# Performance work log

Measured on AMD Instinct MI355X. Metric: run time of the kernel, lower is better.

Reference implementation:

```python
import jax, jax.numpy as jnp
import numpy as np

ATTN_SPLITS = 2
TEMPERATURE = 10000.0

# ---------- split / merge helpers (faithful to split_feature / merge_splits) ----------

def split_cf(x, ns):  # channel-first [b,c,h,w] -> [b*ns*ns, c, h/ns, w/ns]
    b, c, h, w = x.shape
    x = x.reshape(b, c, ns, h // ns, ns, w // ns).transpose(0, 2, 4, 1, 3, 5)
    return x.reshape(b * ns * ns, c, h // ns, w // ns)

def merge_cf(x, ns):  # channel-first inverse
    b, c, h, w = x.shape
    nb = b // (ns * ns)
    x = x.reshape(nb, ns, ns, c, h, w).transpose(0, 3, 1, 4, 2, 5)
    return x.reshape(nb, c, ns * h, ns * w)

def split_cl(x, ns):  # channel-last [b,h,w,c] -> [b*ns*ns, h/ns, w/ns, c]
    b, h, w, c = x.shape
    x = x.reshape(b, ns, h // ns, ns, w // ns, c).transpose(0, 1, 3, 2, 4, 5)
    return x.reshape(b * ns * ns, h // ns, w // ns, c)

def merge_cl(x, ns):  # channel-last inverse
    b, h, w, c = x.shape
    nb = b // (ns * ns)
    x = x.reshape(nb, ns, ns, h, w, c).transpose(0, 1, 3, 2, 4, 5)
    return x.reshape(nb, ns * h, ns * w, c)

# ---------- PositionEmbeddingSine (normalize=True, scale=2*pi) ----------

def pos_embed_sine(h, w, num_pos_feats):
    scale = 2.0 * np.pi
    eps = 1e-6
    ones = jnp.ones((h, w), jnp.float32)
    y_embed = jnp.cumsum(ones, 0)
    x_embed = jnp.cumsum(ones, 1)
    y_embed = y_embed / (y_embed[-1:, :] + eps) * scale
    x_embed = x_embed / (x_embed[:, -1:] + eps) * scale
    dim_t = jnp.arange(num_pos_feats, dtype=jnp.float32)
    dim_t = TEMPERATURE ** (2.0 * jnp.floor(dim_t / 2.0) / num_pos_feats)
    pos_x = x_embed[:, :, None] / dim_t  # [h,w,npf]
    pos_y = y_embed[:, :, None] / dim_t
    pos_x = jnp.stack([jnp.sin(pos_x[:, :, 0::2]), jnp.cos(pos_x[:, :, 1::2])], -1).reshape(h, w, -1)
    pos_y = jnp.stack([jnp.sin(pos_y[:, :, 0::2]), jnp.cos(pos_y[:, :, 1::2])], -1).reshape(h, w, -1)
    pos = jnp.concatenate([pos_y, pos_x], -1)  # [h,w,c]
    return jnp.transpose(pos, (2, 0, 1))[None]  # [1,c,h,w]

def feature_add_position(f0, f1, attn_splits, c):
    if attn_splits > 1:
        f0s = split_cf(f0, attn_splits)
        f1s = split_cf(f1, attn_splits)
        pos = pos_embed_sine(f0s.shape[2], f0s.shape[3], c // 2)
        return merge_cf(f0s + pos, attn_splits), merge_cf(f1s + pos, attn_splits)
    pos = pos_embed_sine(f0.shape[2], f0.shape[3], c // 2)
    return f0 + pos, f1 + pos

# ---------- shifted-window attention mask (static, numpy) ----------

def shift_window_attn_mask(h, w, ns):
    wsh, wsw = h // ns, w // ns
    ssh, ssw = wsh // 2, wsw // 2
    img = np.zeros((h, w), np.float32)
    cnt = 0
    for hs in (slice(0, -wsh), slice(-wsh, -ssh), slice(-ssh, None)):
        for ws in (slice(0, -wsw), slice(-wsw, -ssw), slice(-ssw, None)):
            img[hs, ws] = cnt
            cnt += 1
    m = img.reshape(ns, wsh, ns, wsw).transpose(0, 2, 1, 3).reshape(ns * ns, wsh * wsw)
    am = m[:, None, :] - m[:, :, None]
    am = np.where(am != 0, -100.0, 0.0).astype(np.float32)
    return jnp.asarray(am)  # [ns*ns, N, N]

# ---------- single-head split (shifted) window attention ----------

def split_window_attention(q, k, v, ns, h, w, attn_mask):
    b, _, c = q.shape
    bn = b * ns * ns
    wsh, wsw = h // ns, w // ns
    ssh, ssw = wsh // 2, wsw // 2
    q = q.reshape(b, h, w, c)
    k = k.reshape(b, h, w, c)
    v = v.reshape(b, h, w, c)
    q = jnp.roll(q, (-ssh, -ssw), (1, 2))
    k = jnp.roll(k, (-ssh, -ssw), (1, 2))
    v = jnp.roll(v, (-ssh, -ssw), (1, 2))
    qs = split_cl(q, ns).reshape(bn, -1, c)
    ks = split_cl(k, ns).reshape(bn, -1, c)
    vs = split_cl(v, ns).reshape(bn, -1, c)
    scores = jnp.einsum('bnc,bmc->bnm', qs, ks) / jnp.sqrt(jnp.asarray(c, qs.dtype))
    scores = scores + jnp.tile(attn_mask, (b, 1, 1))
    attn = jax.nn.softmax(scores, axis=-1)
    out = jnp.einsum('bnm,bmc->bnc', attn, vs)
    out = merge_cl(out.reshape(bn, wsh, wsw, c), ns)
    out = jnp.roll(out, (ssh, ssw), (1, 2))
    return out.reshape(b, -1, c)

# ---------- global correlation softmax matching ----------

def global_correlation_softmax(f0, f1):
    b, c, h, w = f0.shape
    f0v = f0.reshape(b, c, -1)  # [b,c,hw]
    f1v = f1.reshape(b, c, -1)
    corr = jnp.einsum('bcn,bcm->bnm', f0v, f1v) / jnp.sqrt(jnp.asarray(c, f0.dtype))
    yy, xx = jnp.meshgrid(jnp.arange(h), jnp.arange(w), indexing='ij')
    grid = jnp.stack([xx, yy], 0).astype(f0.dtype)  # [2,h,w] (x,y)
    gridv = grid.reshape(2, -1).T  # [hw,2]
    prob = jax.nn.softmax(corr, axis=-1)
    corresp = jnp.einsum('bnm,md->bnd', prob, gridv).reshape(b, h, w, 2).transpose(0, 3, 1, 2)
    flow = corresp - grid[None]
    return flow

# ---------- setup & reference ----------

def setup_inputs() -> dict:
    key = jax.random.key(0)
    k0, k1 = jax.random.split(key)
    b, c, h, w = 4, 128, 64, 64
    feature0 = jax.random.normal(k0, (b, c, h, w), jnp.float32)
    feature1 = jax.random.normal(k1, (b, c, h, w), jnp.float32)
    return {'feature0': feature0, 'feature1': feature1}

def reference(feature0, feature1):
    b, c, h, w = feature0.shape
    ns = ATTN_SPLITS
    f0, f1 = feature_add_position(feature0, feature1, ns, c)
    attn_mask = shift_window_attn_mask(h, w, ns)
    q = f0.reshape(b, c, -1).transpose(0, 2, 1)  # [b,hw,c]
    kv = f1.reshape(b, c, -1).transpose(0, 2, 1)
    f0_attn = split_window_attention(q, kv, kv, ns, h, w, attn_mask)  # [b,hw,c]
    f0_attn = f0_attn.transpose(0, 2, 1).reshape(b, c, h, w)
    flow = global_correlation_softmax(f0_attn, f1)  # [b,2,h,w]
    return flow
```

## Files before the change

### kernel.cpp

```cpp
#include <hip/hip_runtime.h>
#include <hip/hip_bf16.h>
#include <math.h>

#define NB 4
#define NC 128
#define NH 64
#define NW 64
#define NHW 4096
#define SCALE 0.08838834764831845f

typedef short bf16x8 __attribute__((ext_vector_type(8)));
typedef float f32x4 __attribute__((ext_vector_type(4)));

__device__ __forceinline__ unsigned bfbits(float f) {
    unsigned u = __float_as_uint(f);
    return (u + 0x7FFFu + ((u >> 16) & 1u)) >> 16;
}
__device__ __forceinline__ unsigned bfpair(float a, float b) {
    return bfbits(a) | (bfbits(b) << 16);
}

__device__ __forceinline__ float posval(int c, int yy, int xx) {
    const float twopi_over_denom = 6.283185307179586f / (32.0f + 1e-6f);
    const int cc = (c < 64) ? c : (c - 64);
    const float e = (float)(((c < 64) ? yy : xx) + 1) * twopi_over_denom;
    const int k = cc >> 1;
    const float arg = e * exp2f(-0.41524101186091903f * (float)k);
    return (cc & 1) ? cosf(arg) : sinf(arg);
}

__global__ __launch_bounds__(256) void pack_kernel(
        const float* __restrict__ f0, const float* __restrict__ f1,
        __hip_bfloat16* __restrict__ F0t, __hip_bfloat16* __restrict__ Bt,
        __hip_bfloat16* __restrict__ Ktw) {
    __shared__ float T[64][129];
    int blk = blockIdx.x;
    const bool isA = blk < 256;
    const float* src = isA ? f0 : f1;
    blk &= 255;
    const int y = blk & 63;
    const int b = blk >> 6;
    const int tid = threadIdx.x;
    const float* s = src + (size_t)b * NC * NHW + y * 64;
    const float sA = isA ? SCALE : 1.0f;
    for (int idx = tid; idx < 64 * NC; idx += 256) {
        const int x = idx & 63, c = idx >> 6;
        T[x][c] = (s[c * NHW + x] + posval(c, y & 31, x & 31)) * sA;
    }
    __syncthreads();
    __hip_bfloat16* dst = isA ? F0t : Bt;
    for (int idx = tid; idx < 512; idx += 256) {
        const int x = idx >> 3, c0 = (idx & 7) * 16;
        const float* tr = &T[x][c0];
        uint4 v0, v1;
        v0.x = bfpair(tr[0], tr[1]);   v0.y = bfpair(tr[2], tr[3]);
        v0.z = bfpair(tr[4], tr[5]);   v0.w = bfpair(tr[6], tr[7]);
        v1.x = bfpair(tr[8], tr[9]);   v1.y = bfpair(tr[10], tr[11]);
        v1.z = bfpair(tr[12], tr[13]); v1.w = bfpair(tr[14], tr[15]);
        __hip_bfloat16* row = dst + ((size_t)b * NHW + y * 64 + x) * NC + c0;
        *reinterpret_cast<uint4*>(row) = v0;
        *reinterpret_cast<uint4*>(row + 8) = v1;
    }
    if (!isA) {
        const int yp = (y + 48) & 63;
        const int wi = yp >> 5, ry = yp & 31;
        const int c = tid >> 1;
        const int wj = tid & 1;
        const int win = b * 4 + wi * 2 + wj;
        unsigned up[16];
        #pragma unroll
        for (int pr = 0; pr < 16; ++pr) {
            const int x0 = ((wj << 5) + 2 * pr + 16) & 63;
            up[pr] = bfpair(T[x0][c], T[x0 + 1][c]);
        }
        __hip_bfloat16* krow = Ktw + ((size_t)win * NC + c) * 1024 + ry * 32;
        uint4* uv = reinterpret_cast<uint4*>(up);
        #pragma unroll
        for (int i = 0; i < 4; ++i)
            *reinterpret_cast<uint4*>(krow + i * 8) = uv[i];
    }
}

__global__ __launch_bounds__(256) void attn_mfma_kernel(
        const __hip_bfloat16* __restrict__ F0t,
        const __hip_bfloat16* __restrict__ Bt,
        const __hip_bfloat16* __restrict__ Ktw,
        __hip_bfloat16* __restrict__ At) {
    __shared__ __align__(16) char lds[73728];
    char* KsB = lds;
    char* VsB = lds + 32768;
    char* Pscr = lds + 65536;
    const int tid = threadIdx.x;
    const int lane = tid & 63;
    const int w = tid >> 6;
    const int l15 = lane & 15;
    const int g = lane >> 4;
    const int blk = blockIdx.x;
    const int win = blk >> 4;
    const int qt = blk & 15;
    const int b = win >> 2, wi = (win >> 1) & 1, wj = win & 1;

    const char* Btb = (const char*)(Bt + (size_t)b * NHW * NC);
    const char* Vsrc = (const char*)(Ktw + (size_t)win * NC * 1024);

    bf16x8 qf[4];
    {
        const int tok = qt * 64 + w * 16 + l15;
        const int yo = ((wi << 5) + (tok >> 5) + 16) & 63;
        const int xo = ((wj << 5) + (tok & 31) + 16) & 63;
        const __hip_bfloat16* qrow =
            F0t + ((size_t)b * NHW + yo * 64 + xo) * NC + g * 8;
        #pragma unroll
        for (int kk = 0; kk < 4; ++kk)
            qf[kk] = *reinterpret_cast<const bf16x8*>(qrow + kk * 32);
    }

    const int reg_q = (wi ? (qt < 8 ? 1 : 2) : 0) * 3
                    + (wj ? ((w & 1) == 0 ? 1 : 2) : 0);

    auto stageK = [&](int buf, int kt) {
        char* dst = KsB + buf * 16384;
        #pragma unroll
        for (int it = 0; it < 4; ++it) {
            const int obase = w * 4096 + it * 1024;
            const int row = w * 16 + it * 4 + (lane >> 4);
            const int tok = kt * 64 + row;
            const int yo = ((wi << 5) + (tok >> 5) + 16) & 63;
            const int xo = ((wj << 5) + (tok & 31) + 16) & 63;
            const char* src = Btb + (yo * 64 + xo) * 256 +
                              (((lane & 15) * 16) ^ ((row & 7) << 4));
            __builtin_amdgcn_global_load_lds(
                (const __attribute__((address_space(1))) void*)src,
                (__attribute__((address_space(3))) void*)(dst + obase), 16, 0, 0);
        }
    };
    auto stageV = [&](int buf, int kt) {
        char* dst = VsB + buf * 16384;
        #pragma unroll
        for (int it = 0; it < 4; ++it) {
            const int obase = w * 4096 + it * 1024;
            const int o = obase + lane * 16;
            const int crow = o >> 7;
            const int off = o & 127;
            __builtin_amdgcn_global_load_lds(
                (const __attribute__((address_space(1))) void*)(Vsrc + crow * 2048 + kt * 128 + (off ^ ((crow & 7) << 4))),
                (__attribute__((address_space(3))) void*)(dst + obase), 16, 0, 0);
        }
    };

    f32x4 oacc[8] = {{0,0,0,0},{0,0,0,0},{0,0,0,0},{0,0,0,0},
                     {0,0,0,0},{0,0,0,0},{0,0,0,0},{0,0,0,0}};
    float zacc = 0.f;

    stageK(0, 0); stageV(0, 0);
    __syncthreads();

    for (int kt = 0; kt < 16; ++kt) {
        const int buf = kt & 1;
        if (kt < 15) { stageK(buf ^ 1, kt + 1); stageV(buf ^ 1, kt + 1); }

        const char* kb = KsB + buf * 16384;
        f32x4 sacc[4] = {{0,0,0,0},{0,0,0,0},{0,0,0,0},{0,0,0,0}};
        #pragma unroll
        for (int kk = 0; kk < 4; ++kk) {
            #pragma unroll
            for (int msub = 0; msub < 4; ++msub) {
                const int byte = msub * 4096 + l15 * 256 + ((kk * 64 + g * 16) ^ ((l15 & 7) << 4));
                bf16x8 kf = *reinterpret_cast<const bf16x8*>(kb + byte);
                sacc[msub] = __builtin_amdgcn_mfma_f32_16x16x32_bf16(kf, qf[kk], sacc[msub], 0, 0, 0);
            }
        }

        const int rk_row = (wi ? (kt < 8 ? 1 : 2) : 0) * 3;
        char* pw = Pscr + w * 2048;
        #pragma unroll
        for (int msub = 0; msub < 4; ++msub) {
            const int rk = rk_row + (wj ? ((msub & 1) == 0 ? 1 : 2) : 0);
            const bool ok = (rk == reg_q);
            const float p0 = ok ? __expf(sacc[msub][0]) : 0.f;
            const float p1 = ok ? __expf(sacc[msub][1]) : 0.f;
            const float p2 = ok ? __expf(sacc[msub][2]) : 0.f;
            const float p3 = ok ? __expf(sacc[msub][3]) : 0.f;
            zacc += (p0 + p1) + (p2 + p3);
            *reinterpret_cast<unsigned*>(pw + l15 * 128 + ((msub * 32 + g * 8 + 0) ^ ((l15 & 7) << 4))) = bfpair(p0, p1);
            *reinterpret_cast<unsigned*>(pw + l15 * 128 + ((msub * 32 + g * 8 + 4) ^ ((l15 & 7) << 4))) = bfpair(p2, p3);
        }
        bf16x8 pf[2];
        #pragma unroll
        for (int kk = 0; kk < 2; ++kk)
            pf[kk] = *reinterpret_cast<const bf16x8*>(pw + l15 * 128 + ((kk * 64 + g * 16) ^ ((l15 & 7) << 4)));

        const char* vb = VsB + buf * 16384;
        #pragma unroll
        for (int kk = 0; kk < 2; ++kk) {
            #pragma unroll
            for (int co = 0; co < 8; ++co) {
                const int byte = (co * 16 + l15) * 128 + ((kk * 64 + g * 16) ^ ((l15 & 7) << 4));
                bf16x8 vf = *reinterpret_cast<const bf16x8*>(vb + byte);
                oacc[co] = __builtin_amdgcn_mfma_f32_16x16x32_bf16(pf[kk], vf, oacc[co], 0, 0, 0);
            }
        }
        __syncthreads();
    }

    float z = zacc;
    z += __shfl_xor(z, 16);
    z += __shfl_xor(z, 32);

    unsigned short* olds = reinterpret_cast<unsigned short*>(lds + w * 4096);
    #pragma unroll
    for (int r = 0; r < 4; ++r) {
        const float zi = SCALE / __shfl(z, g * 4 + r);
        #pragma unroll
        for (int co = 0; co < 8; ++co)
            olds[(g * 4 + r) * 128 + co * 16 + l15] = (unsigned short)bfbits(oacc[co][r] * zi);
    }

    const int qloc = lane >> 2;
    const int c0 = (lane & 3) * 32;
    const int tok = qt * 64 + w * 16 + qloc;
    const int yo = ((wi << 5) + (tok >> 5) + 16) & 63;
    const int xo = ((wj << 5) + (tok & 31) + 16) & 63;
    __hip_bfloat16* arow = At + ((size_t)b * NHW + yo * 64 + xo) * NC + c0;
    #pragma unroll
    for (int i = 0; i < 4; ++i) {
        int4 v = *reinterpret_cast<const int4*>(olds + qloc * 128 + c0 + i * 8);
        *reinterpret_cast<int4*>(arow + i * 8) = v;
    }
}

__global__ __launch_bounds__(256) void corr_part_kernel(
        const __hip_bfloat16* __restrict__ At,
        const __hip_bfloat16* __restrict__ Bt,
        float4* __restrict__ part) {
    __shared__ __hip_bfloat16 Bs[2][64 * 128];
    const int tid = threadIdx.x;
    const int lane = tid & 63;
    const int w = tid >> 6;
    const int blk = blockIdx.x;
    const int ms = blk & 7;
    const int nt = (blk >> 3) & 31;
    const int b = blk >> 8;
    const int l15 = lane & 15;
    const int g = lane >> 4;
    const int n0 = nt * 128 + w * 32;

    const __hip_bfloat16* Ab = At + (size_t)b * NHW * NC;
    const __hip_bfloat16* Bb = Bt + (size_t)b * NHW * NC;

    bf16x8 afrag[2][4];
    #pragma unroll
    for (int s = 0; s < 2; ++s) {
        const __hip_bfloat16* arow = Ab + (size_t)(n0 + s * 16 + l15) * NC + g * 8;
        #pragma unroll
        for (int kk = 0; kk < 4; ++kk)
            afrag[s][kk] = *reinterpret_cast<const bf16x8*>(arow + kk * 32);
    }

    auto stage = [&](int buf, int mtile) {
        const char* srcbase = reinterpret_cast<const char*>(Bb + (size_t)mtile * 64 * NC);
        #pragma unroll
        for (int it = 0; it < 4; ++it) {
            const int obase = w * 4096 + it * 1024;
            const int o = obase + lane * 16;
            const int row = o >> 8;
            const int off = o & 255;
            const char* src = srcbase + row * 256 + (off ^ ((row & 7) << 4));
            __builtin_amdgcn_global_load_lds(
                (const __attribute__((address_space(1))) void*)src,
                (__attribute__((address_space(3))) void*)((char*)&Bs[buf][0] + obase),
                16, 0, 0);
        }
    };

    f32x4 rl[2] = {{0,0,0,0},{0,0,0,0}};
    f32x4 rsm[2] = {{0,0,0,0},{0,0,0,0}};
    f32x4 rsy[2] = {{0,0,0,0},{0,0,0,0}};

    stage(0, ms * 8);
    __syncthreads();

    for (int mt = 0; mt < 8; ++mt) {
        const int buf = mt & 1;
        if (mt < 7) stage(buf ^ 1, ms * 8 + mt + 1);

        f32x4 acc[2][4] = {{{0,0,0,0},{0,0,0,0},{0,0,0,0},{0,0,0,0}},
                           {{0,0,0,0},{0,0,0,0},{0,0,0,0},{0,0,0,0}}};
        const char* base = (const char*)&Bs[buf][0];
        #pragma unroll
        for (int kk = 0; kk < 4; ++kk) {
            #pragma unroll
            for (int msub = 0; msub < 4; ++msub) {
                const int byte = msub * 4096 + l15 * 256 +
                                 ((kk * 64 + g * 16) ^ ((l15 & 7) << 4));
                bf16x8 bfrag = *reinterpret_cast<const bf16x8*>(base + byte);
                acc[0][msub] = __builtin_amdgcn_mfma_f32_16x16x32_bf16(
                    afrag[0][kk], bfrag, acc[0][msub], 0, 0, 0);
                acc[1][msub] = __builtin_amdgcn_mfma_f32_16x16x32_bf16(
                    afrag[1][kk], bfrag, acc[1][msub], 0, 0, 0);
            }
        }
        const float y0 = (float)(ms * 8 + mt);
        #pragma unroll
        for (int s = 0; s < 2; ++s) {
            #pragma unroll
            for (int r = 0; r < 4; ++r) {
                float p0 = __expf(acc[s][0][r]);
                float p1 = __expf(acc[s][1][r]);
                float p2 = __expf(acc[s][2][r]);
                float p3 = __expf(acc[s][3][r]);
                float ts = (p0 + p1) + (p2 + p3);
                rl[s][r]  += ts;
                rsy[s][r] += y0 * ts;
                rsm[s][r] += fmaf(3.f, p3, fmaf(2.f, p2, p1));
            }
        }
        __syncthreads();
    }

    const float xl = (float)l15;
    #pragma unroll
    for (int s = 0; s < 2; ++s) {
        #pragma unroll
        for (int r = 0; r < 4; ++r) {
            float a  = rl[s][r];
            float sx = xl * rl[s][r] + 16.f * rsm[s][r];
            float sy = rsy[s][r];
            #pragma unroll
            for (int m = 1; m < 16; m <<= 1) {
                a  += __shfl_xor(a, m);
                sx += __shfl_xor(sx, m);
                sy += __shfl_xor(sy, m);
            }
            if (l15 == 0) {
                const int n = n0 + s * 16 + g * 4 + r;
                part[((size_t)b * NHW + n) * 8 + ms] = make_float4(a, sx, sy, 0.f);
            }
        }
    }
}

__global__ __launch_bounds__(256) void finalize_kernel(
        const float4* __restrict__ part, float* __restrict__ out) {
    const int idx = blockIdx.x * 256 + threadIdx.x;
    if (idx >= NB * NHW) return;
    const int n = idx & (NHW - 1);
    const int b = idx >> 12;
    float l = 0.f, sx = 0.f, sy = 0.f;
    #pragma unroll
    for (int i = 0; i < 8; ++i) {
        float4 p = part[(size_t)idx * 8 + i];
        l += p.x; sx += p.y; sy += p.z;
    }
    const float inv = 1.0f / l;
    out[(size_t)b * 2 * NHW + n]       = sx * inv - (float)(n & 63);
    out[(size_t)b * 2 * NHW + NHW + n] = sy * inv - (float)(n >> 6);
}

extern "C" void kernel_launch(void* const* d_in, const int* in_sizes, int n_in,
                              void* d_out, int out_size, void* d_ws, size_t ws_size,
                              hipStream_t stream) {
    const float* f0 = (const float*)d_in[0];
    const float* f1 = (const float*)d_in[1];
    __hip_bfloat16* F0t = (__hip_bfloat16*)d_ws;
    __hip_bfloat16* Bt  = F0t + (size_t)NB * NHW * NC;
    __hip_bfloat16* Ktw = Bt  + (size_t)NB * NHW * NC;
    __hip_bfloat16* At  = Ktw + (size_t)16 * NC * 1024;
    float4* part = (float4*)(At + (size_t)NB * NHW * NC);
    float* out = (float*)d_out;

    pack_kernel<<<512, 256, 0, stream>>>(f0, f1, F0t, Bt, Ktw);
    attn_mfma_kernel<<<256, 256, 0, stream>>>(F0t, Bt, Ktw, At);
    corr_part_kernel<<<1024, 256, 0, stream>>>(At, Bt, part);
    finalize_kernel<<<64, 256, 0, stream>>>(part, out);
}
```

Measured before the change: 74.75 us.

## Split attention keys across two blocks and precompute positional embedding table

```diff
diff --git a/kernel.cpp b/kernel.cpp
--- a/kernel.cpp
+++ b/kernel.cpp
@@ -20,17 +20,25 @@
     return bfbits(a) | (bfbits(b) << 16);
 }
 
-__device__ __forceinline__ float posval(int c, int yy, int xx) {
-    const float twopi_over_denom = 6.283185307179586f / (32.0f + 1e-6f);
-    const int cc = (c < 64) ? c : (c - 64);
-    const float e = (float)(((c < 64) ? yy : xx) + 1) * twopi_over_denom;
-    const int k = cc >> 1;
-    const float arg = e * exp2f(-0.41524101186091903f * (float)k);
-    return (cc & 1) ? cosf(arg) : sinf(arg);
+__global__ __launch_bounds__(256) void pos_kernel(float* __restrict__ pos) {
+    int idx = blockIdx.x * 256 + threadIdx.x;
+    if (idx >= NC * 32 * 32) return;
+    int x = idx & 31;
+    int y = (idx >> 5) & 31;
+    int c = idx >> 10;
+    const float twopi = 6.283185307179586f;
+    const float denom = 32.0f + 1e-6f;
+    int cc = (c < 64) ? c : (c - 64);
+    float e = (c < 64) ? (float)(y + 1) : (float)(x + 1);
+    e = e * (twopi / denom);
+    int k = cc >> 1;
+    float arg = e * exp2f(-0.41524101186091903f * (float)k);
+    pos[idx] = (cc & 1) ? cosf(arg) : sinf(arg);
 }
 
 __global__ __launch_bounds__(256) void pack_kernel(
         const float* __restrict__ f0, const float* __restrict__ f1,
+        const float* __restrict__ pos,
         __hip_bfloat16* __restrict__ F0t, __hip_bfloat16* __restrict__ Bt,
         __hip_bfloat16* __restrict__ Ktw) {
     __shared__ float T[64][129];
@@ -45,7 +53,7 @@
     const float sA = isA ? SCALE : 1.0f;
     for (int idx = tid; idx < 64 * NC; idx += 256) {
         const int x = idx & 63, c = idx >> 6;
-        T[x][c] = (s[c * NHW + x] + posval(c, y & 31, x & 31)) * sA;
+        T[x][c] = (s[c * NHW + x] + pos[(c << 10) + ((y & 31) << 5) + (x & 31)]) * sA;
     }
     __syncthreads();
     __hip_bfloat16* dst = isA ? F0t : Bt;
@@ -85,7 +93,8 @@
         const __hip_bfloat16* __restrict__ F0t,
         const __hip_bfloat16* __restrict__ Bt,
         const __hip_bfloat16* __restrict__ Ktw,
-        __hip_bfloat16* __restrict__ At) {
+        float* __restrict__ Opart,
+        float* __restrict__ Zpart) {
     __shared__ __align__(16) char lds[73728];
     char* KsB = lds;
     char* VsB = lds + 32768;
@@ -96,8 +105,9 @@
     const int l15 = lane & 15;
     const int g = lane >> 4;
     const int blk = blockIdx.x;
-    const int win = blk >> 4;
-    const int qt = blk & 15;
+    const int ks = blk & 1;
+    const int qt = (blk >> 1) & 15;
+    const int win = blk >> 5;
     const int b = win >> 2, wi = (win >> 1) & 1, wj = win & 1;
 
     const char* Btb = (const char*)(Bt + (size_t)b * NHW * NC);
@@ -118,13 +128,13 @@
     const int reg_q = (wi ? (qt < 8 ? 1 : 2) : 0) * 3
                     + (wj ? ((w & 1) == 0 ? 1 : 2) : 0);
 
-    auto stageK = [&](int buf, int kt) {
+    auto stageK = [&](int buf, int ktg) {
         char* dst = KsB + buf * 16384;
         #pragma unroll
         for (int it = 0; it < 4; ++it) {
             const int obase = w * 4096 + it * 1024;
             const int row = w * 16 + it * 4 + (lane >> 4);
-            const int tok = kt * 64 + row;
+            const int tok = ktg * 64 + row;
             const int yo = ((wi << 5) + (tok >> 5) + 16) & 63;
             const int xo = ((wj << 5) + (tok & 31) + 16) & 63;
             const char* src = Btb + (yo * 64 + xo) * 256 +
@@ -134,7 +144,7 @@
                 (__attribute__((address_space(3))) void*)(dst + obase), 16, 0, 0);
         }
     };
-    auto stageV = [&](int buf, int kt) {
+    auto stageV = [&](int buf, int ktg) {
         char* dst = VsB + buf * 16384;
         #pragma unroll
         for (int it = 0; it < 4; ++it) {
@@ -143,7 +153,7 @@
             const int crow = o >> 7;
             const int off = o & 127;
             __builtin_amdgcn_global_load_lds(
-                (const __attribute__((address_space(1))) void*)(Vsrc + crow * 2048 + kt * 128 + (off ^ ((crow & 7) << 4))),
+                (const __attribute__((address_space(1))) void*)(Vsrc + crow * 2048 + ktg * 128 + (off ^ ((crow & 7) << 4))),
                 (__attribute__((address_space(3))) void*)(dst + obase), 16, 0, 0);
         }
     };
@@ -152,12 +162,13 @@
                      {0,0,0,0},{0,0,0,0},{0,0,0,0},{0,0,0,0}};
     float zacc = 0.f;
 
-    stageK(0, 0); stageV(0, 0);
+    stageK(0, ks * 8); stageV(0, ks * 8);
     __syncthreads();
 
-    for (int kt = 0; kt < 16; ++kt) {
+    for (int kt = 0; kt < 8; ++kt) {
+        const int ktg = ks * 8 + kt;
         const int buf = kt & 1;
-        if (kt < 15) { stageK(buf ^ 1, kt + 1); stageV(buf ^ 1, kt + 1); }
+        if (kt < 7) { stageK(buf ^ 1, ktg + 1); stageV(buf ^ 1, ktg + 1); }
 
         const char* kb = KsB + buf * 16384;
         f32x4 sacc[4] = {{0,0,0,0},{0,0,0,0},{0,0,0,0},{0,0,0,0}};
@@ -171,7 +182,7 @@
             }
         }
 
-        const int rk_row = (wi ? (kt < 8 ? 1 : 2) : 0) * 3;
+        const int rk_row = (wi ? (ktg < 8 ? 1 : 2) : 0) * 3;
         char* pw = Pscr + w * 2048;
         #pragma unroll
         for (int msub = 0; msub < 4; ++msub) {
@@ -207,25 +218,49 @@
     z += __shfl_xor(z, 16);
     z += __shfl_xor(z, 32);
 
-    unsigned short* olds = reinterpret_cast<unsigned short*>(lds + w * 4096);
+    float* of = reinterpret_cast<float*>(lds + w * 8192);
     #pragma unroll
     for (int r = 0; r < 4; ++r) {
-        const float zi = SCALE / __shfl(z, g * 4 + r);
         #pragma unroll
         for (int co = 0; co < 8; ++co)
-            olds[(g * 4 + r) * 128 + co * 16 + l15] = (unsigned short)bfbits(oacc[co][r] * zi);
-    }
-
-    const int qloc = lane >> 2;
-    const int c0 = (lane & 3) * 32;
-    const int tok = qt * 64 + w * 16 + qloc;
+            of[(g * 4 + r) * 128 + co * 16 + l15] = oacc[co][r];
+    }
+    const size_t obase = ((size_t)blk * 64 + w * 16) * 128;
+    #pragma unroll
+    for (int j = 0; j < 8; ++j) {
+        const int flat = j * 256 + lane * 4;
+        *reinterpret_cast<float4*>(&Opart[obase + flat]) =
+            *reinterpret_cast<const float4*>(&of[flat]);
+    }
+    if (lane < 16) Zpart[blk * 64 + w * 16 + lane] = z;
+}
+
+__global__ __launch_bounds__(256) void attn_fin_kernel(
+        const float* __restrict__ Opart, const float* __restrict__ Zpart,
+        __hip_bfloat16* __restrict__ At) {
+    const int t = blockIdx.x * 256 + threadIdx.x;
+    if (t >= 16 * 1024) return;
+    const int win = t >> 10, tok = t & 1023;
+    const int qt = tok >> 6, rowloc = tok & 63;
+    const int blk0 = win * 32 + qt * 2;
+    const float z = Zpart[blk0 * 64 + rowloc] + Zpart[(blk0 + 1) * 64 + rowloc];
+    const float zi = SCALE / z;
+    const float4* o0 = reinterpret_cast<const float4*>(Opart + ((size_t)blk0 * 64 + rowloc) * 128);
+    const float4* o1 = o0 + (64 * 128 / 4);
+    const int b = win >> 2, wi = (win >> 1) & 1, wj = win & 1;
     const int yo = ((wi << 5) + (tok >> 5) + 16) & 63;
     const int xo = ((wj << 5) + (tok & 31) + 16) & 63;
-    __hip_bfloat16* arow = At + ((size_t)b * NHW + yo * 64 + xo) * NC + c0;
-    #pragma unroll
-    for (int i = 0; i < 4; ++i) {
-        int4 v = *reinterpret_cast<const int4*>(olds + qloc * 128 + c0 + i * 8);
-        *reinterpret_cast<int4*>(arow + i * 8) = v;
+    __hip_bfloat16* arow = At + ((size_t)b * NHW + yo * 64 + xo) * NC;
+    #pragma unroll
+    for (int i = 0; i < 16; ++i) {
+        float4 a = o0[i * 2], b4 = o0[i * 2 + 1];
+        float4 c = o1[i * 2], d4 = o1[i * 2 + 1];
+        uint4 v;
+        v.x = bfpair((a.x + c.x) * zi, (a.y + c.y) * zi);
+        v.y = bfpair((a.z + c.z) * zi, (a.w + c.w) * zi);
+        v.z = bfpair((b4.x + d4.x) * zi, (b4.y + d4.y) * zi);
+        v.w = bfpair((b4.z + d4.z) * zi, (b4.w + d4.w) * zi);
+        *reinterpret_cast<uint4*>(arow + i * 8) = v;
     }
 }
 
@@ -362,15 +397,20 @@
                               hipStream_t stream) {
     const float* f0 = (const float*)d_in[0];
     const float* f1 = (const float*)d_in[1];
-    __hip_bfloat16* F0t = (__hip_bfloat16*)d_ws;
+    float* pos = (float*)d_ws;
+    __hip_bfloat16* F0t = (__hip_bfloat16*)(pos + 131072);
     __hip_bfloat16* Bt  = F0t + (size_t)NB * NHW * NC;
     __hip_bfloat16* Ktw = Bt  + (size_t)NB * NHW * NC;
     __hip_bfloat16* At  = Ktw + (size_t)16 * NC * 1024;
     float4* part = (float4*)(At + (size_t)NB * NHW * NC);
+    float* Opart = (float*)(part + (size_t)NB * NHW * 8);
+    float* Zpart = Opart + (size_t)512 * 64 * 128;
     float* out = (float*)d_out;
 
-    pack_kernel<<<512, 256, 0, stream>>>(f0, f1, F0t, Bt, Ktw);
-    attn_mfma_kernel<<<256, 256, 0, stream>>>(F0t, Bt, Ktw, At);
+    pos_kernel<<<512, 256, 0, stream>>>(pos);
+    pack_kernel<<<512, 256, 0, stream>>>(f0, f1, pos, F0t, Bt, Ktw);
+    attn_mfma_kernel<<<512, 256, 0, stream>>>(F0t, Bt, Ktw, Opart, Zpart);
+    attn_fin_kernel<<<64, 256, 0, stream>>>(Opart, Zpart, At);
     corr_part_kernel<<<1024, 256, 0, stream>>>(At, Bt, part);
     finalize_kernel<<<64, 256, 0, stream>>>(part, out);
 }
```

Result: slower. 82.59 us (+10.5%).

## Precompute positional table in separate kernel and double correlation tile per wave

Applied to the files above, without the earlier changes.

```diff
diff --git a/kernel.cpp b/kernel.cpp
--- a/kernel.cpp
+++ b/kernel.cpp
@@ -20,17 +20,25 @@
     return bfbits(a) | (bfbits(b) << 16);
 }
 
-__device__ __forceinline__ float posval(int c, int yy, int xx) {
-    const float twopi_over_denom = 6.283185307179586f / (32.0f + 1e-6f);
-    const int cc = (c < 64) ? c : (c - 64);
-    const float e = (float)(((c < 64) ? yy : xx) + 1) * twopi_over_denom;
-    const int k = cc >> 1;
-    const float arg = e * exp2f(-0.41524101186091903f * (float)k);
-    return (cc & 1) ? cosf(arg) : sinf(arg);
+__global__ __launch_bounds__(256) void pos_kernel(float* __restrict__ pos) {
+    int idx = blockIdx.x * 256 + threadIdx.x;
+    if (idx >= NC * 32 * 32) return;
+    int x = idx & 31;
+    int y = (idx >> 5) & 31;
+    int c = idx >> 10;
+    const float twopi = 6.283185307179586f;
+    const float denom = 32.0f + 1e-6f;
+    int cc = (c < 64) ? c : (c - 64);
+    float e = (c < 64) ? (float)(y + 1) : (float)(x + 1);
+    e = e * (twopi / denom);
+    int k = cc >> 1;
+    float arg = e * exp2f(-0.41524101186091903f * (float)k);
+    pos[idx] = (cc & 1) ? cosf(arg) : sinf(arg);
 }
 
 __global__ __launch_bounds__(256) void pack_kernel(
         const float* __restrict__ f0, const float* __restrict__ f1,
+        const float* __restrict__ pos,
         __hip_bfloat16* __restrict__ F0t, __hip_bfloat16* __restrict__ Bt,
         __hip_bfloat16* __restrict__ Ktw) {
     __shared__ float T[64][129];
@@ -45,7 +53,7 @@
     const float sA = isA ? SCALE : 1.0f;
     for (int idx = tid; idx < 64 * NC; idx += 256) {
         const int x = idx & 63, c = idx >> 6;
-        T[x][c] = (s[c * NHW + x] + posval(c, y & 31, x & 31)) * sA;
+        T[x][c] = (s[c * NHW + x] + pos[(c << 10) + ((y & 31) << 5) + (x & 31)]) * sA;
     }
     __syncthreads();
     __hip_bfloat16* dst = isA ? F0t : Bt;
@@ -229,7 +237,7 @@
     }
 }
 
-__global__ __launch_bounds__(256) void corr_part_kernel(
+__global__ __launch_bounds__(256, 2) void corr_part_kernel(
         const __hip_bfloat16* __restrict__ At,
         const __hip_bfloat16* __restrict__ Bt,
         float4* __restrict__ part) {
@@ -239,18 +247,18 @@
     const int w = tid >> 6;
     const int blk = blockIdx.x;
     const int ms = blk & 7;
-    const int nt = (blk >> 3) & 31;
-    const int b = blk >> 8;
+    const int nt = (blk >> 3) & 15;
+    const int b = blk >> 7;
     const int l15 = lane & 15;
     const int g = lane >> 4;
-    const int n0 = nt * 128 + w * 32;
+    const int n0 = nt * 256 + w * 64;
 
     const __hip_bfloat16* Ab = At + (size_t)b * NHW * NC;
     const __hip_bfloat16* Bb = Bt + (size_t)b * NHW * NC;
 
-    bf16x8 afrag[2][4];
-    #pragma unroll
-    for (int s = 0; s < 2; ++s) {
+    bf16x8 afrag[4][4];
+    #pragma unroll
+    for (int s = 0; s < 4; ++s) {
         const __hip_bfloat16* arow = Ab + (size_t)(n0 + s * 16 + l15) * NC + g * 8;
         #pragma unroll
         for (int kk = 0; kk < 4; ++kk)
@@ -273,9 +281,9 @@
         }
     };
 
-    f32x4 rl[2] = {{0,0,0,0},{0,0,0,0}};
-    f32x4 rsm[2] = {{0,0,0,0},{0,0,0,0}};
-    f32x4 rsy[2] = {{0,0,0,0},{0,0,0,0}};
+    f32x4 rl[4]  = {{0,0,0,0},{0,0,0,0},{0,0,0,0},{0,0,0,0}};
+    f32x4 rsm[4] = {{0,0,0,0},{0,0,0,0},{0,0,0,0},{0,0,0,0}};
+    f32x4 rsy[4] = {{0,0,0,0},{0,0,0,0},{0,0,0,0},{0,0,0,0}};
 
     stage(0, ms * 8);
     __syncthreads();
@@ -284,7 +292,9 @@
         const int buf = mt & 1;
         if (mt < 7) stage(buf ^ 1, ms * 8 + mt + 1);
 
-        f32x4 acc[2][4] = {{{0,0,0,0},{0,0,0,0},{0,0,0,0},{0,0,0,0}},
+        f32x4 acc[4][4] = {{{0,0,0,0},{0,0,0,0},{0,0,0,0},{0,0,0,0}},
+                           {{0,0,0,0},{0,0,0,0},{0,0,0,0},{0,0,0,0}},
+                           {{0,0,0,0},{0,0,0,0},{0,0,0,0},{0,0,0,0}},
                            {{0,0,0,0},{0,0,0,0},{0,0,0,0},{0,0,0,0}}};
         const char* base = (const char*)&Bs[buf][0];
         #pragma unroll
@@ -294,15 +304,15 @@
                 const int byte = msub * 4096 + l15 * 256 +
                                  ((kk * 64 + g * 16) ^ ((l15 & 7) << 4));
                 bf16x8 bfrag = *reinterpret_cast<const bf16x8*>(base + byte);
-                acc[0][msub] = __builtin_amdgcn_mfma_f32_16x16x32_bf16(
-                    afrag[0][kk], bfrag, acc[0][msub], 0, 0, 0);
-                acc[1][msub] = __builtin_amdgcn_mfma_f32_16x16x32_bf16(
-                    afrag[1][kk], bfrag, acc[1][msub], 0, 0, 0);
+                #pragma unroll
+                for (int s = 0; s < 4; ++s)
+                    acc[s][msub] = __builtin_amdgcn_mfma_f32_16x16x32_bf16(
+                        afrag[s][kk], bfrag, acc[s][msub], 0, 0, 0);
             }
         }
         const float y0 = (float)(ms * 8 + mt);
         #pragma unroll
-        for (int s = 0; s < 2; ++s) {
+        for (int s = 0; s < 4; ++s) {
             #pragma unroll
             for (int r = 0; r < 4; ++r) {
                 float p0 = __expf(acc[s][0][r]);
@@ -320,7 +330,7 @@
 
     const float xl = (float)l15;
     #pragma unroll
-    for (int s = 0; s < 2; ++s) {
+    for (int s = 0; s < 4; ++s) {
         #pragma unroll
         for (int r = 0; r < 4; ++r) {
             float a  = rl[s][r];
@@ -362,15 +372,17 @@
                               hipStream_t stream) {
     const float* f0 = (const float*)d_in[0];
     const float* f1 = (const float*)d_in[1];
-    __hip_bfloat16* F0t = (__hip_bfloat16*)d_ws;
+    float* pos = (float*)d_ws;
+    __hip_bfloat16* F0t = (__hip_bfloat16*)(pos + 131072);
     __hip_bfloat16* Bt  = F0t + (size_t)NB * NHW * NC;
     __hip_bfloat16* Ktw = Bt  + (size_t)NB * NHW * NC;
     __hip_bfloat16* At  = Ktw + (size_t)16 * NC * 1024;
     float4* part = (float4*)(At + (size_t)NB * NHW * NC);
     float* out = (float*)d_out;
 
-    pack_kernel<<<512, 256, 0, stream>>>(f0, f1, F0t, Bt, Ktw);
+    pos_kernel<<<512, 256, 0, stream>>>(pos);
+    pack_kernel<<<512, 256, 0, stream>>>(f0, f1, pos, F0t, Bt, Ktw);
     attn_mfma_kernel<<<256, 256, 0, stream>>>(F0t, Bt, Ktw, At);
-    corr_part_kernel<<<1024, 256, 0, stream>>>(At, Bt, part);
+    corr_part_kernel<<<512, 256, 0, stream>>>(At, Bt, part);
     finalize_kernel<<<64, 256, 0, stream>>>(part, out);
 }
```

New measurement: 70.96 us. 5.1% less time.
